# Optimization experiments

Hardware: AMD Instinct MI355X
Metric: run time of the kernel (lower is better)

Reference implementation:

```python
import jax, jax.numpy as jnp
import numpy as np

DIM = 2048
HEAD_DIM = 64
N_HEADS = 16
N_KV_HEADS = 4
RANK = 8
ALPHA = 16
LORA_SCALE = ALPHA / RANK  # 2.0
SEQ = 2048
BATCH = 1
ROPE_THETA = 10000.0


def setup_inputs() -> dict:
    key = jax.random.key(0)
    ks = jax.random.split(key, 12)
    std = 0.02
    x = jax.random.normal(ks[0], (BATCH, SEQ, DIM), dtype=jnp.float32)
    # rope tables: (SEQ, HEAD_DIM//2, 2) = (cos, sin)
    inv_freq = 1.0 / (ROPE_THETA ** (jnp.arange(0, HEAD_DIM, 2, dtype=jnp.float32) / HEAD_DIM))
    ang = jnp.arange(SEQ, dtype=jnp.float32)[:, None] * inv_freq[None, :]
    freq_cis = jnp.stack([jnp.cos(ang), jnp.sin(ang)], axis=-1)
    mk = lambda k, shp: (jax.random.normal(k, shp, dtype=jnp.float32) * std)
    return {
        "x": x,
        "freq_cis": freq_cis,
        "wq": mk(ks[1], (HEAD_DIM, DIM)),
        "wq_a": mk(ks[2], (RANK, DIM)),
        "wq_b": mk(ks[3], (N_HEADS * HEAD_DIM, RANK)),
        "wk": mk(ks[4], (HEAD_DIM, DIM)),
        "wk_a": mk(ks[5], (RANK, DIM)),
        "wk_b": mk(ks[6], (N_KV_HEADS * HEAD_DIM, RANK)),
        "wv": mk(ks[7], (HEAD_DIM, DIM)),
        "wv_a": mk(ks[8], (RANK, DIM)),
        "wv_b": mk(ks[9], (N_KV_HEADS * HEAD_DIM, RANK)),
        "wo": mk(ks[10], (DIM, HEAD_DIM)),
        "wo_share": mk(ks[11], (DIM, N_HEADS * HEAD_DIM)),
    }


def _shared_plus_lora(x, w_base, w_a, w_b, n_heads):
    # base: single head (B,S,HEAD_DIM) broadcast across heads; LoRA adds per-head delta
    base = jnp.einsum('bsd,hd->bsh', x, w_base)                    # (B,S,Dh)
    delta = jnp.einsum('bsr,or->bso', jnp.einsum('bsd,rd->bsr', x, w_a), w_b) * LORA_SCALE
    B, S, _ = x.shape
    delta = delta.reshape(B, S, n_heads, HEAD_DIM)
    return base[:, :, None, :] + delta                             # (B,S,H,Dh)


def _rope(t, freq_cis):
    # t: (B,S,H,Dh); freq_cis: (S, Dh//2, 2)
    B, S, H, D = t.shape
    tr = t.reshape(B, S, H, D // 2, 2)
    cos = freq_cis[:, None, :, 0]  # (S,1,Dh//2)
    sin = freq_cis[:, None, :, 1]
    xr, xi = tr[..., 0], tr[..., 1]
    out = jnp.stack([xr * cos - xi * sin, xr * sin + xi * cos], axis=-1)
    return out.reshape(B, S, H, D)


def reference(x, freq_cis, wq, wq_a, wq_b, wk, wk_a, wk_b, wv, wv_a, wv_b, wo, wo_share):
    B, S, _ = x.shape
    g = N_HEADS // N_KV_HEADS
    xq = _shared_plus_lora(x, wq, wq_a, wq_b, N_HEADS)      # (B,S,H,Dh)
    xk = _shared_plus_lora(x, wk, wk_a, wk_b, N_KV_HEADS)   # (B,S,Hkv,Dh)
    xv = _shared_plus_lora(x, wv, wv_a, wv_b, N_KV_HEADS)
    xq = _rope(xq, freq_cis[:S])
    xk = _rope(xk, freq_cis[:S])
    # GQA attention without materializing repeat_kv: group q heads per kv head
    q = xq.reshape(B, S, N_KV_HEADS, g, HEAD_DIM)
    scale = 1.0 / jnp.sqrt(jnp.asarray(HEAD_DIM, dtype=x.dtype))
    scores = jnp.einsum('bskgd,btkd->bkgst', q, xk) * scale  # (B,Hkv,g,S,S)
    causal = jnp.tril(jnp.ones((S, S), dtype=bool))
    scores = jnp.where(causal, scores, jnp.asarray(-jnp.inf, dtype=scores.dtype))
    p = jax.nn.softmax(scores, axis=-1)
    out = jnp.einsum('bkgst,btkd->bskgd', p, xv).reshape(B, S, N_HEADS, HEAD_DIM)
    # output projection: shared base applied per-head then summed + LoRA-style shared delta
    base = jnp.einsum('bshd,ed->bse', out, wo)
    delta = jnp.einsum('bsf,ef->bse', out.reshape(B, S, N_HEADS * HEAD_DIM), wo_share)
    return base + delta
```

## Files before the change

### kernel.cpp

```cpp
#include <hip/hip_runtime.h>
#include <hip/hip_bf16.h>

#define DEV __device__ __forceinline__

typedef unsigned short u16;
typedef __attribute__((ext_vector_type(8))) short short8;
typedef __attribute__((ext_vector_type(4))) float f32x4;
typedef __attribute__((ext_vector_type(16))) float f32x16;

DEV u16 f2bf(float f) {
  union { float f; unsigned u; } v; v.f = f;
  unsigned r = v.u + 0x7FFFu + ((v.u >> 16) & 1u);
  return (u16)(r >> 16);
}

DEV float bf2f(u16 b) {
  union { unsigned u; float f; } v; v.u = ((unsigned)b) << 16; return v.f;
}

DEV unsigned cvtpk(float lo, float hi) {
  unsigned r;
  asm("v_cvt_pk_bf16_f32 %0, %1, %2" : "=v"(r) : "v"(lo), "v"(hi));
  return r;
}

DEV void async_ld16(const u16* g, u16* l) {
  __builtin_amdgcn_global_load_lds((__attribute__((address_space(1))) void*)g,
                                   (__attribute__((address_space(3))) void*)l,
                                   16, 0, 0);
}

DEV f32x4 mfma16(short8 a, short8 b, f32x4 c) {
  return __builtin_amdgcn_mfma_f32_16x16x32_bf16(a, b, c, 0, 0, 0);
}
DEV f32x16 mfma32(short8 a, short8 b, f32x16 c) {
  return __builtin_amdgcn_mfma_f32_32x32x16_bf16(a, b, c, 0, 0, 0);
}

DEV short8 mkfrag(unsigned w0, unsigned w1, unsigned w2, unsigned w3) {
  union { unsigned u[4]; short8 s; } u;
  u.u[0] = w0; u.u[1] = w1; u.u[2] = w2; u.u[3] = w3;
  return u.s;
}

DEV short8 lds_rd(const u16* buf, int row, int colb) {
  return *(const short8*)((const char*)buf + row*128 + (colb ^ ((row & 7) << 4)));
}

#define QSCALE (0.125f * 1.4426950408889634f)

__global__ __launch_bounds__(256) void k_prep(const float* __restrict__ x,
    const float* __restrict__ wq, const float* __restrict__ wk,
    const float* __restrict__ wv, const float* __restrict__ wqa,
    const float* __restrict__ wka, const float* __restrict__ wva,
    const float* __restrict__ wo, const float* __restrict__ wos,
    u16* __restrict__ xb, u16* __restrict__ W1, u16* __restrict__ Weff) {
  const int bid = blockIdx.x;
  if (bid < 1024) {
    int i = bid*256 + threadIdx.x;
    for (; i < 1048576; i += 1024*256) {
      float4 v = ((const float4*)x)[i];
      ushort4 o;
      o.x = f2bf(v.x); o.y = f2bf(v.y); o.z = f2bf(v.z); o.w = f2bf(v.w);
      ((ushort4*)xb)[i] = o;
    }
  } else if (bid < 1280) {
    const int row = bid - 1024;
    const float* src = nullptr; float sc = 1.f;
    if (row < 64)       { src = wq  + row*2048;       sc = QSCALE; }
    else if (row < 128) { src = wk  + (row-64)*2048;  }
    else if (row < 192) { src = wv  + (row-128)*2048; }
    else if (row < 200) { src = wqa + (row-192)*2048; sc = 2.f*QSCALE; }
    else if (row < 208) { src = wka + (row-200)*2048; sc = 2.f; }
    else if (row < 216) { src = wva + (row-208)*2048; sc = 2.f; }
    for (int c = threadIdx.x; c < 2048; c += 256)
      W1[row*2048 + c] = src ? f2bf(src[c]*sc) : (u16)0;
  } else {
    const int e = bid - 1280;
    for (int f = threadIdx.x; f < 1024; f += 256)
      Weff[e*1024 + f] = f2bf(wos[e*1024 + f] + wo[e*64 + (f & 63)]);
  }
}

template<int BM, int BN, bool OBF16>
__global__ __launch_bounds__(512)
void k_gemm_bt(const u16* __restrict__ A, const u16* __restrict__ B,
               void* __restrict__ Cv, int M, int N, int K, int kslice) {
  constexpr int NWC = (BN >= 128) ? 4 : 2;
  constexpr int NWR = 8 / NWC;
  constexpr int WM = BM / NWR, WN = BN / NWC;
  constexpr int FM = WM/16, FN = WN/16;
  __shared__ u16 As[BM*64];
  __shared__ u16 Bs[BN*64];
  const int tid = threadIdx.x;
  const int w = tid >> 6, l = tid & 63;
  const int wm = (w / NWC)*WM, wn = (w % NWC)*WN;
  const int tm = blockIdx.y*BM, tn = blockIdx.x*BN;
  const int k0 = blockIdx.z * kslice;
  const int sr = (w << 3) + (l >> 3);
  const int sc = (((l & 7) ^ (l >> 3)) << 3);
  const int la = l & 15, lg = l >> 4;

  f32x4 acc[FM][FN];
#pragma unroll
  for (int i = 0; i < FM; ++i)
#pragma unroll
    for (int j = 0; j < FN; ++j) acc[i][j] = (f32x4){0.f,0.f,0.f,0.f};

  const int nk = kslice >> 6;
  for (int kt = 0; kt < nk; ++kt) {
    const int kk = k0 + (kt << 6);
#pragma unroll
    for (int j = 0; j < BM/64; ++j)
      async_ld16(A + (size_t)(tm + j*64 + sr)*K + kk + sc, &As[(j*64 + w*8)*64]);
#pragma unroll
    for (int j = 0; j < BN/64; ++j)
      async_ld16(B + (size_t)(tn + j*64 + sr)*K + kk + sc, &Bs[(j*64 + w*8)*64]);
    __syncthreads();
    short8 af[FM][2], bfr[FN][2];
#pragma unroll
    for (int mi = 0; mi < FM; ++mi)
#pragma unroll
      for (int ks = 0; ks < 2; ++ks)
        af[mi][ks] = lds_rd(As, wm + mi*16 + la, ks*64 + lg*16);
#pragma unroll
    for (int ni = 0; ni < FN; ++ni)
#pragma unroll
      for (int ks = 0; ks < 2; ++ks)
        bfr[ni][ks] = lds_rd(Bs, wn + ni*16 + la, ks*64 + lg*16);
#pragma unroll
    for (int ks = 0; ks < 2; ++ks)
#pragma unroll
      for (int mi = 0; mi < FM; ++mi)
#pragma unroll
        for (int ni = 0; ni < FN; ++ni)
          acc[mi][ni] = mfma16(af[mi][ks], bfr[ni][ks], acc[mi][ni]);
    __syncthreads();
  }
#pragma unroll
  for (int mi = 0; mi < FM; ++mi)
#pragma unroll
    for (int ni = 0; ni < FN; ++ni) {
      const int r0 = tm + wm + mi*16 + lg*4;
      const int cc = tn + wn + ni*16 + la;
      if constexpr (OBF16) {
        u16* C = (u16*)Cv + (size_t)blockIdx.z * M * N;
#pragma unroll
        for (int r = 0; r < 4; ++r)
          C[(size_t)(r0 + r)*N + cc] = f2bf(acc[mi][ni][r]);
      } else {
        float* C = (float*)Cv + (size_t)blockIdx.z * M * N;
#pragma unroll
        for (int r = 0; r < 4; ++r)
          C[(size_t)(r0 + r)*N + cc] = acc[mi][ni][r];
      }
    }
}

__global__ __launch_bounds__(256)
void k_expand(const u16* __restrict__ proj, const float* __restrict__ wqb,
              const float* __restrict__ wkb, const float* __restrict__ wvb,
              const float* __restrict__ freq, u16* __restrict__ Q,
              u16* __restrict__ Kb, u16* __restrict__ Vt) {
  __shared__ float prs[256];
  const int s = blockIdx.x;
  {
    const int c = threadIdx.x;
    const u16* p0 = proj + s*256;
    float acc = 0.f;
#pragma unroll
    for (int k = 0; k < 8; ++k) acc += bf2f(p0[c + k*524288]);
    prs[c] = acc;
  }
  __syncthreads();
  const int d = threadIdx.x & 63;
  const int w = threadIdx.x >> 6;
  const float cs = freq[s*64 + (d & 62)];
  const float sn = freq[s*64 + (d & 62) + 1];
#pragma unroll
  for (int pass = 0; pass < 6; ++pass) {
    const int slot = pass*4 + w;
    int bcol, tb; const float* wb;
    if (slot < 16)      { bcol = 0;   tb = 192; wb = wqb + (slot*64 + d)*8; }
    else if (slot < 20) { bcol = 64;  tb = 200; wb = wkb + ((slot-16)*64 + d)*8; }
    else                { bcol = 128; tb = 208; wb = wvb + ((slot-20)*64 + d)*8; }
    float val = prs[bcol + d];
#pragma unroll
    for (int r = 0; r < 8; ++r) val += prs[tb + r] * wb[r];
    if (slot < 20) {
      float partner = __shfl_xor(val, 1);
      val = (d & 1) ? (partner*sn + val*cs) : (val*cs - partner*sn);
    }
    u16 o = f2bf(val);
    if (slot < 16)      Q [((size_t)slot*2048 + s)*64 + d] = o;
    else if (slot < 20) Kb[((size_t)(slot-16)*2048 + s)*64 + d] = o;
    else                Vt[(size_t)(slot-20)*131072 + (size_t)d*2048 + s] = o;
  }
}

__global__ __launch_bounds__(256, 4)
void k_attn(const u16* __restrict__ Q, const u16* __restrict__ Kb,
            const u16* __restrict__ Vt, u16* __restrict__ O) {
  __shared__ __align__(16) char smem[33792];
  const int w = threadIdx.x >> 6, l = threadIdx.x & 63;
  const int bid = blockIdx.x;
  const int h = bid & 15, kh = h >> 2;
  const int z = bid >> 4;
  const int a = z & 15, b = z >> 4;
  const int qs = (b << 4) | ((b & 1) ? (15 - a) : a);
  const int q0 = qs*32;
  const int lq = l & 31, hh = l >> 5;
  const int qg = q0 + lq;

  u16* kbuf = (u16*)(smem + w*8192);
  u16* vbuf = (u16*)(smem + w*8192 + 4096);

  const u16* Qh = Q  + (size_t)h *131072;
  const u16* Kh = Kb + (size_t)kh*131072;
  const u16* Vh = Vt + (size_t)kh*131072;

  short8 bq[4];
#pragma unroll
  for (int ks = 0; ks < 4; ++ks)
    bq[ks] = *(const short8*)&Qh[qg*64 + ks*16 + hh*8];

  f32x16 acc0, acc1;
#pragma unroll
  for (int r = 0; r < 16; ++r) { acc0[r] = 0.f; acc1[r] = 0.f; }
  float lsum = 0.f;
  const float SM = 20.f;

  const int nt = qs + 1;

#define STAGE_K(T0)                                                       \
  {                                                                       \
    const int t0_ = (T0);                                                 \
    _Pragma("unroll")                                                     \
    for (int j = 0; j < 4; ++j) {                                         \
      const int c = j*64 + l;                                             \
      const int row = c >> 3, e = (c & 7) ^ (row & 7);                    \
      async_ld16(Kh + (size_t)(t0_ + row)*64 + e*8, kbuf + j*512);        \
    }                                                                     \
  }
#define STAGE_V(T0)                                                       \
  {                                                                       \
    const int t0_ = (T0);                                                 \
    _Pragma("unroll")                                                     \
    for (int j = 0; j < 4; ++j) {                                         \
      const int c = j*64 + l;                                             \
      const int row = c >> 3, e = (c & 7) ^ (row & 7);                    \
      const int dd = row + (e >> 2)*32;                                   \
      async_ld16(Vh + (size_t)dd*2048 + t0_ + (e & 3)*8, vbuf + j*512);   \
    }                                                                     \
  }

  if (w < nt) { STAGE_K(w*32); STAGE_V(w*32); }

  for (int tt = w; tt < nt; tt += 4) {
    asm volatile("s_waitcnt vmcnt(0)" ::: "memory");
    __builtin_amdgcn_sched_barrier(0);
    short8 ak[4];
#pragma unroll
    for (int ks = 0; ks < 4; ++ks)
      ak[ks] = lds_rd(kbuf, lq, ks*32 + hh*16);
    asm volatile("s_waitcnt lgkmcnt(0)" ::: "memory");
    __builtin_amdgcn_sched_barrier(0);
    if (tt + 4 < nt) STAGE_K((tt + 4)*32);

    f32x16 s;
#pragma unroll
    for (int r = 0; r < 16; ++r) s[r] = 0.f;
    __builtin_amdgcn_s_setprio(1);
#pragma unroll
    for (int ks = 0; ks < 4; ++ks)
      s = mfma32(ak[ks], bq[ks], s);
    __builtin_amdgcn_s_setprio(0);

    const int t0 = tt*32;
    if (t0 + 31 > q0) {
#pragma unroll
      for (int r = 0; r < 16; ++r) {
        const int tl = (r & 3) + ((r >> 2) << 3) + (hh << 2);
        if (t0 + tl > qg) s[r] = -1e30f;
      }
    }

    short8 av[2][2];
#pragma unroll
    for (int dh = 0; dh < 2; ++dh)
#pragma unroll
      for (int k2 = 0; k2 < 2; ++k2)
        av[dh][k2] = lds_rd(vbuf, lq, (dh*4 + k2*2 + hh)*16);

    unsigned cw[4][2];
    float psum = 0.f;
#pragma unroll
    for (int rq = 0; rq < 4; ++rq) {
      float a0 = exp2f(s[4*rq+0] - SM), a1 = exp2f(s[4*rq+1] - SM);
      float a2 = exp2f(s[4*rq+2] - SM), a3 = exp2f(s[4*rq+3] - SM);
      psum += (a0 + a1) + (a2 + a3);
      cw[rq][0] = cvtpk(a0, a1); cw[rq][1] = cvtpk(a2, a3);
    }
    lsum += psum;

    asm volatile("s_waitcnt lgkmcnt(0)" ::: "memory");
    __builtin_amdgcn_sched_barrier(0);
    if (tt + 4 < nt) STAGE_V((tt + 4)*32);

    unsigned y00 = __shfl_xor(hh ? cw[0][0] : cw[1][0], 32);
    unsigned y01 = __shfl_xor(hh ? cw[0][1] : cw[1][1], 32);
    unsigned y10 = __shfl_xor(hh ? cw[2][0] : cw[3][0], 32);
    unsigned y11 = __shfl_xor(hh ? cw[2][1] : cw[3][1], 32);
    short8 p0 = hh ? mkfrag(y00, y01, cw[1][0], cw[1][1])
                   : mkfrag(cw[0][0], cw[0][1], y00, y01);
    short8 p1 = hh ? mkfrag(y10, y11, cw[3][0], cw[3][1])
                   : mkfrag(cw[2][0], cw[2][1], y10, y11);

    __builtin_amdgcn_s_setprio(1);
    acc0 = mfma32(av[0][0], p0, acc0);
    acc1 = mfma32(av[1][0], p0, acc1);
    acc0 = mfma32(av[0][1], p1, acc0);
    acc1 = mfma32(av[1][1], p1, acc1);
    __builtin_amdgcn_s_setprio(0);
  }
#undef STAGE_K
#undef STAGE_V

  __syncthreads();
  float* comb = (float*)smem;
  u16* scr = (u16*)(smem + 26624);
  if (w > 0) {
    float* cb = comb + ((w-1)*64 + l)*33;
#pragma unroll
    for (int r = 0; r < 16; ++r) { cb[r] = acc0[r]; cb[16+r] = acc1[r]; }
    cb[32] = lsum;
  }
  __syncthreads();
  if (w == 0) {
#pragma unroll
    for (int j = 0; j < 3; ++j) {
      const float* cb = comb + (j*64 + l)*33;
#pragma unroll
      for (int r = 0; r < 16; ++r) { acc0[r] += cb[r]; acc1[r] += cb[16+r]; }
      lsum += cb[32];
    }
    lsum += __shfl_xor(lsum, 32);
    const float inv = 1.f / lsum;
#pragma unroll
    for (int dt = 0; dt < 2; ++dt)
#pragma unroll
      for (int rq = 0; rq < 4; ++rq) {
        float v0 = (dt ? acc1[4*rq+0] : acc0[4*rq+0]) * inv;
        float v1 = (dt ? acc1[4*rq+1] : acc0[4*rq+1]) * inv;
        float v2 = (dt ? acc1[4*rq+2] : acc0[4*rq+2]) * inv;
        float v3 = (dt ? acc1[4*rq+3] : acc0[4*rq+3]) * inv;
        const int dby = dt*64 + rq*16 + hh*8;
        const int by = lq*128 + (dby ^ ((lq & 7) << 4));
        *(unsigned*)((char*)scr + by)     = cvtpk(v0, v1);
        *(unsigned*)((char*)scr + by + 4) = cvtpk(v2, v3);
      }
#pragma unroll
    for (int qq = 0; qq < 4; ++qq) {
      const int qrow = qq*8 + (l >> 3);
      const int by = qrow*128 + (((l & 7) << 4) ^ ((qrow & 7) << 4));
      short8 v = *(const short8*)((const char*)scr + by);
      *(short8*)&O[(size_t)(q0 + qrow)*1024 + h*64 + (l & 7)*8] = v;
    }
  }
}

extern "C" void kernel_launch(void* const* d_in, const int* in_sizes, int n_in,
                              void* d_out, int out_size, void* d_ws, size_t ws_size,
                              hipStream_t stream) {
  const float* x    = (const float*)d_in[0];
  const float* freq = (const float*)d_in[1];
  const float* wq   = (const float*)d_in[2];
  const float* wqa  = (const float*)d_in[3];
  const float* wqb  = (const float*)d_in[4];
  const float* wk   = (const float*)d_in[5];
  const float* wka  = (const float*)d_in[6];
  const float* wkb  = (const float*)d_in[7];
  const float* wv   = (const float*)d_in[8];
  const float* wva  = (const float*)d_in[9];
  const float* wvb  = (const float*)d_in[10];
  const float* wo   = (const float*)d_in[11];
  const float* wos  = (const float*)d_in[12];

  char* ws = (char*)d_ws;
  u16*  x_bf = (u16*)ws;
  u16*  Qb   = (u16*)ws;
  u16*  Kbuf = (u16*)(ws + (4u<<20));
  u16*  Vtb  = (u16*)(ws + (5u<<20));
  u16*  W1   = (u16*)(ws + (8u<<20));
  u16*  Weff = (u16*)(ws + (9u<<20));
  u16*  proj = (u16*)(ws + (13u<<20));
  u16*  Obf  = (u16*)(ws + (13u<<20));

  k_prep    <<<3328, 256, 0, stream>>>(x, wq, wk, wv, wqa, wka, wva, wo, wos,
                                       x_bf, W1, Weff);
  k_gemm_bt<128,64,true><<<dim3(4,16,8), 512, 0, stream>>>(x_bf, W1, proj,
                                                           2048, 256, 2048, 256);
  k_expand  <<<dim3(2048), 256, 0, stream>>>(proj, wqb, wkb, wvb, freq, Qb, Kbuf, Vtb);
  k_attn    <<<dim3(1024), 256, 0, stream>>>(Qb, Kbuf, Vtb, Obf);
  k_gemm_bt<64,128,false><<<dim3(16,32,1), 512, 0, stream>>>(Obf, Weff, (float*)d_out,
                                                             2048, 2048, 1024, 1024);
}
```

Measured before the change: 77.62 us.

## Pair causal query tiles per block and split KV across eight waves

The attention kernel now launches 512 blocks of 512 threads. Each block handles two query tiles, z and 63-z, in sequence, so every block carries the same causal workload, and eight waves split the KV tiles instead of four. Partial accumulators are combined with a three-step tree reduction through shared memory. This removes load imbalance between causal tiles and the tail effect, at the cost of 64KB of LDS per block, more barriers, and possibly lower occupancy.

```diff
diff --git a/kernel.cpp b/kernel.cpp
--- a/kernel.cpp
+++ b/kernel.cpp
@@ -198,19 +198,15 @@
   }
 }
 
-__global__ __launch_bounds__(256, 4)
+__global__ __launch_bounds__(512, 4)
 void k_attn(const u16* __restrict__ Q, const u16* __restrict__ Kb,
             const u16* __restrict__ Vt, u16* __restrict__ O) {
-  __shared__ __align__(16) char smem[33792];
+  __shared__ __align__(16) char smem[65536];
   const int w = threadIdx.x >> 6, l = threadIdx.x & 63;
   const int bid = blockIdx.x;
   const int h = bid & 15, kh = h >> 2;
   const int z = bid >> 4;
-  const int a = z & 15, b = z >> 4;
-  const int qs = (b << 4) | ((b & 1) ? (15 - a) : a);
-  const int q0 = qs*32;
   const int lq = l & 31, hh = l >> 5;
-  const int qg = q0 + lq;
 
   u16* kbuf = (u16*)(smem + w*8192);
   u16* vbuf = (u16*)(smem + w*8192 + 4096);
@@ -218,19 +214,7 @@
   const u16* Qh = Q  + (size_t)h *131072;
   const u16* Kh = Kb + (size_t)kh*131072;
   const u16* Vh = Vt + (size_t)kh*131072;
-
-  short8 bq[4];
-#pragma unroll
-  for (int ks = 0; ks < 4; ++ks)
-    bq[ks] = *(const short8*)&Qh[qg*64 + ks*16 + hh*8];
-
-  f32x16 acc0, acc1;
-#pragma unroll
-  for (int r = 0; r < 16; ++r) { acc0[r] = 0.f; acc1[r] = 0.f; }
-  float lsum = 0.f;
   const float SM = 20.f;
-
-  const int nt = qs + 1;
 
 #define STAGE_K(T0)                                                       \
   {                                                                       \
@@ -254,119 +238,163 @@
     }                                                                     \
   }
 
-  if (w < nt) { STAGE_K(w*32); STAGE_V(w*32); }
-
-  for (int tt = w; tt < nt; tt += 4) {
-    asm volatile("s_waitcnt vmcnt(0)" ::: "memory");
-    __builtin_amdgcn_sched_barrier(0);
-    short8 ak[4];
+#pragma unroll 1
+  for (int ph = 0; ph < 2; ++ph) {
+    const int qs = ph ? (63 - z) : z;
+    const int q0 = qs*32;
+    const int qg = q0 + lq;
+    const int nt = qs + 1;
+
+    short8 bq[4];
 #pragma unroll
     for (int ks = 0; ks < 4; ++ks)
-      ak[ks] = lds_rd(kbuf, lq, ks*32 + hh*16);
-    asm volatile("s_waitcnt lgkmcnt(0)" ::: "memory");
-    __builtin_amdgcn_sched_barrier(0);
-    if (tt + 4 < nt) STAGE_K((tt + 4)*32);
-
-    f32x16 s;
-#pragma unroll
-    for (int r = 0; r < 16; ++r) s[r] = 0.f;
-    __builtin_amdgcn_s_setprio(1);
-#pragma unroll
-    for (int ks = 0; ks < 4; ++ks)
-      s = mfma32(ak[ks], bq[ks], s);
-    __builtin_amdgcn_s_setprio(0);
-
-    const int t0 = tt*32;
-    if (t0 + 31 > q0) {
-#pragma unroll
-      for (int r = 0; r < 16; ++r) {
-        const int tl = (r & 3) + ((r >> 2) << 3) + (hh << 2);
-        if (t0 + tl > qg) s[r] = -1e30f;
+      bq[ks] = *(const short8*)&Qh[qg*64 + ks*16 + hh*8];
+
+    f32x16 acc0, acc1;
+#pragma unroll
+    for (int r = 0; r < 16; ++r) { acc0[r] = 0.f; acc1[r] = 0.f; }
+    float lsum = 0.f;
+
+    if (w < nt) { STAGE_K(w*32); STAGE_V(w*32); }
+
+    for (int tt = w; tt < nt; tt += 8) {
+      asm volatile("s_waitcnt vmcnt(0)" ::: "memory");
+      __builtin_amdgcn_sched_barrier(0);
+      short8 ak[4];
+#pragma unroll
+      for (int ks = 0; ks < 4; ++ks)
+        ak[ks] = lds_rd(kbuf, lq, ks*32 + hh*16);
+      asm volatile("s_waitcnt lgkmcnt(0)" ::: "memory");
+      __builtin_amdgcn_sched_barrier(0);
+      if (tt + 8 < nt) STAGE_K((tt + 8)*32);
+
+      f32x16 s;
+#pragma unroll
+      for (int r = 0; r < 16; ++r) s[r] = 0.f;
+      __builtin_amdgcn_s_setprio(1);
+#pragma unroll
+      for (int ks = 0; ks < 4; ++ks)
+        s = mfma32(ak[ks], bq[ks], s);
+      __builtin_amdgcn_s_setprio(0);
+
+      const int t0 = tt*32;
+      if (t0 + 31 > q0) {
+#pragma unroll
+        for (int r = 0; r < 16; ++r) {
+          const int tl = (r & 3) + ((r >> 2) << 3) + (hh << 2);
+          if (t0 + tl > qg) s[r] = -1e30f;
+        }
       }
-    }
-
-    short8 av[2][2];
-#pragma unroll
-    for (int dh = 0; dh < 2; ++dh)
-#pragma unroll
-      for (int k2 = 0; k2 < 2; ++k2)
-        av[dh][k2] = lds_rd(vbuf, lq, (dh*4 + k2*2 + hh)*16);
-
-    unsigned cw[4][2];
-    float psum = 0.f;
-#pragma unroll
-    for (int rq = 0; rq < 4; ++rq) {
-      float a0 = exp2f(s[4*rq+0] - SM), a1 = exp2f(s[4*rq+1] - SM);
-      float a2 = exp2f(s[4*rq+2] - SM), a3 = exp2f(s[4*rq+3] - SM);
-      psum += (a0 + a1) + (a2 + a3);
-      cw[rq][0] = cvtpk(a0, a1); cw[rq][1] = cvtpk(a2, a3);
-    }
-    lsum += psum;
-
-    asm volatile("s_waitcnt lgkmcnt(0)" ::: "memory");
-    __builtin_amdgcn_sched_barrier(0);
-    if (tt + 4 < nt) STAGE_V((tt + 4)*32);
-
-    unsigned y00 = __shfl_xor(hh ? cw[0][0] : cw[1][0], 32);
-    unsigned y01 = __shfl_xor(hh ? cw[0][1] : cw[1][1], 32);
-    unsigned y10 = __shfl_xor(hh ? cw[2][0] : cw[3][0], 32);
-    unsigned y11 = __shfl_xor(hh ? cw[2][1] : cw[3][1], 32);
-    short8 p0 = hh ? mkfrag(y00, y01, cw[1][0], cw[1][1])
-                   : mkfrag(cw[0][0], cw[0][1], y00, y01);
-    short8 p1 = hh ? mkfrag(y10, y11, cw[3][0], cw[3][1])
-                   : mkfrag(cw[2][0], cw[2][1], y10, y11);
-
-    __builtin_amdgcn_s_setprio(1);
-    acc0 = mfma32(av[0][0], p0, acc0);
-    acc1 = mfma32(av[1][0], p0, acc1);
-    acc0 = mfma32(av[0][1], p1, acc0);
-    acc1 = mfma32(av[1][1], p1, acc1);
-    __builtin_amdgcn_s_setprio(0);
+
+      short8 av[2][2];
+#pragma unroll
+      for (int dh = 0; dh < 2; ++dh)
+#pragma unroll
+        for (int k2 = 0; k2 < 2; ++k2)
+          av[dh][k2] = lds_rd(vbuf, lq, (dh*4 + k2*2 + hh)*16);
+
+      unsigned cw[4][2];
+      float psum = 0.f;
+#pragma unroll
+      for (int rq = 0; rq < 4; ++rq) {
+        float a0 = exp2f(s[4*rq+0] - SM), a1 = exp2f(s[4*rq+1] - SM);
+        float a2 = exp2f(s[4*rq+2] - SM), a3 = exp2f(s[4*rq+3] - SM);
+        psum += (a0 + a1) + (a2 + a3);
+        cw[rq][0] = cvtpk(a0, a1); cw[rq][1] = cvtpk(a2, a3);
+      }
+      lsum += psum;
+
+      asm volatile("s_waitcnt lgkmcnt(0)" ::: "memory");
+      __builtin_amdgcn_sched_barrier(0);
+      if (tt + 8 < nt) STAGE_V((tt + 8)*32);
+
+      unsigned y00 = __shfl_xor(hh ? cw[0][0] : cw[1][0], 32);
+      unsigned y01 = __shfl_xor(hh ? cw[0][1] : cw[1][1], 32);
+      unsigned y10 = __shfl_xor(hh ? cw[2][0] : cw[3][0], 32);
+      unsigned y11 = __shfl_xor(hh ? cw[2][1] : cw[3][1], 32);
+      short8 p0 = hh ? mkfrag(y00, y01, cw[1][0], cw[1][1])
+                     : mkfrag(cw[0][0], cw[0][1], y00, y01);
+      short8 p1 = hh ? mkfrag(y10, y11, cw[3][0], cw[3][1])
+                     : mkfrag(cw[2][0], cw[2][1], y10, y11);
+
+      __builtin_amdgcn_s_setprio(1);
+      acc0 = mfma32(av[0][0], p0, acc0);
+      acc1 = mfma32(av[1][0], p0, acc1);
+      acc0 = mfma32(av[0][1], p1, acc0);
+      acc1 = mfma32(av[1][1], p1, acc1);
+      __builtin_amdgcn_s_setprio(0);
+    }
+
+    __syncthreads();
+    float* comb = (float*)smem;
+    u16* scr = (u16*)(smem + 33792);
+    if (w >= 4) {
+      float* cb = comb + ((w-4)*64 + l)*33;
+#pragma unroll
+      for (int r = 0; r < 16; ++r) { cb[r] = acc0[r]; cb[16+r] = acc1[r]; }
+      cb[32] = lsum;
+    }
+    __syncthreads();
+    if (w < 4) {
+      const float* cb = comb + (w*64 + l)*33;
+#pragma unroll
+      for (int r = 0; r < 16; ++r) { acc0[r] += cb[r]; acc1[r] += cb[16+r]; }
+      lsum += cb[32];
+    }
+    __syncthreads();
+    if (w == 2 || w == 3) {
+      float* cb = comb + ((w-2)*64 + l)*33;
+#pragma unroll
+      for (int r = 0; r < 16; ++r) { cb[r] = acc0[r]; cb[16+r] = acc1[r]; }
+      cb[32] = lsum;
+    }
+    __syncthreads();
+    if (w < 2) {
+      const float* cb = comb + (w*64 + l)*33;
+#pragma unroll
+      for (int r = 0; r < 16; ++r) { acc0[r] += cb[r]; acc1[r] += cb[16+r]; }
+      lsum += cb[32];
+    }
+    __syncthreads();
+    if (w == 1) {
+      float* cb = comb + l*33;
+#pragma unroll
+      for (int r = 0; r < 16; ++r) { cb[r] = acc0[r]; cb[16+r] = acc1[r]; }
+      cb[32] = lsum;
+    }
+    __syncthreads();
+    if (w == 0) {
+      const float* cb = comb + l*33;
+#pragma unroll
+      for (int r = 0; r < 16; ++r) { acc0[r] += cb[r]; acc1[r] += cb[16+r]; }
+      lsum += cb[32];
+      lsum += __shfl_xor(lsum, 32);
+      const float inv = 1.f / lsum;
+#pragma unroll
+      for (int dt = 0; dt < 2; ++dt)
+#pragma unroll
+        for (int rq = 0; rq < 4; ++rq) {
+          float v0 = (dt ? acc1[4*rq+0] : acc0[4*rq+0]) * inv;
+          float v1 = (dt ? acc1[4*rq+1] : acc0[4*rq+1]) * inv;
+          float v2 = (dt ? acc1[4*rq+2] : acc0[4*rq+2]) * inv;
+          float v3 = (dt ? acc1[4*rq+3] : acc0[4*rq+3]) * inv;
+          const int dby = dt*64 + rq*16 + hh*8;
+          const int by = lq*128 + (dby ^ ((lq & 7) << 4));
+          *(unsigned*)((char*)scr + by)     = cvtpk(v0, v1);
+          *(unsigned*)((char*)scr + by + 4) = cvtpk(v2, v3);
+        }
+#pragma unroll
+      for (int qq = 0; qq < 4; ++qq) {
+        const int qrow = qq*8 + (l >> 3);
+        const int by = qrow*128 + (((l & 7) << 4) ^ ((qrow & 7) << 4));
+        short8 v = *(const short8*)((const char*)scr + by);
+        *(short8*)&O[(size_t)(q0 + qrow)*1024 + h*64 + (l & 7)*8] = v;
+      }
+    }
+    __syncthreads();
   }
 #undef STAGE_K
 #undef STAGE_V
-
-  __syncthreads();
-  float* comb = (float*)smem;
-  u16* scr = (u16*)(smem + 26624);
-  if (w > 0) {
-    float* cb = comb + ((w-1)*64 + l)*33;
-#pragma unroll
-    for (int r = 0; r < 16; ++r) { cb[r] = acc0[r]; cb[16+r] = acc1[r]; }
-    cb[32] = lsum;
-  }
-  __syncthreads();
-  if (w == 0) {
-#pragma unroll
-    for (int j = 0; j < 3; ++j) {
-      const float* cb = comb + (j*64 + l)*33;
-#pragma unroll
-      for (int r = 0; r < 16; ++r) { acc0[r] += cb[r]; acc1[r] += cb[16+r]; }
-      lsum += cb[32];
-    }
-    lsum += __shfl_xor(lsum, 32);
-    const float inv = 1.f / lsum;
-#pragma unroll
-    for (int dt = 0; dt < 2; ++dt)
-#pragma unroll
-      for (int rq = 0; rq < 4; ++rq) {
-        float v0 = (dt ? acc1[4*rq+0] : acc0[4*rq+0]) * inv;
-        float v1 = (dt ? acc1[4*rq+1] : acc0[4*rq+1]) * inv;
-        float v2 = (dt ? acc1[4*rq+2] : acc0[4*rq+2]) * inv;
-        float v3 = (dt ? acc1[4*rq+3] : acc0[4*rq+3]) * inv;
-        const int dby = dt*64 + rq*16 + hh*8;
-        const int by = lq*128 + (dby ^ ((lq & 7) << 4));
-        *(unsigned*)((char*)scr + by)     = cvtpk(v0, v1);
-        *(unsigned*)((char*)scr + by + 4) = cvtpk(v2, v3);
-      }
-#pragma unroll
-    for (int qq = 0; qq < 4; ++qq) {
-      const int qrow = qq*8 + (l >> 3);
-      const int by = qrow*128 + (((l & 7) << 4) ^ ((qrow & 7) << 4));
-      short8 v = *(const short8*)((const char*)scr + by);
-      *(short8*)&O[(size_t)(q0 + qrow)*1024 + h*64 + (l & 7)*8] = v;
-    }
-  }
 }
 
 extern "C" void kernel_launch(void* const* d_in, const int* in_sizes, int n_in,
@@ -401,7 +429,7 @@
   k_gemm_bt<128,64,true><<<dim3(4,16,8), 512, 0, stream>>>(x_bf, W1, proj,
                                                            2048, 256, 2048, 256);
   k_expand  <<<dim3(2048), 256, 0, stream>>>(proj, wqb, wkb, wvb, freq, Qb, Kbuf, Vtb);
-  k_attn    <<<dim3(1024), 256, 0, stream>>>(Qb, Kbuf, Vtb, Obf);
+  k_attn    <<<dim3(512), 512, 0, stream>>>(Qb, Kbuf, Vtb, Obf);
   k_gemm_bt<64,128,false><<<dim3(16,32,1), 512, 0, stream>>>(Obf, Weff, (float*)d_out,
                                                              2048, 2048, 1024, 1024);
 }
```

Result: slower. 101.0 us (+30.1%).
